# Optimization experiments

Hardware: AMD Instinct MI355X
Metric: run time of the kernel (lower is better)

## Reference

```python
import jax, jax.numpy as jnp
import numpy as np

NUM_HEADS = 12
SIZE_PER_HEAD = 64
NEG_INF = -10000.0


def setup_inputs() -> dict:
    key = jax.random.key(0)
    k1, k2, k3, k4 = jax.random.split(key, 4)
    B, S, D = 2, 2048, 768
    x = jax.random.normal(k1, (B, S, D), dtype=jnp.float32)
    mask = jax.random.randint(k2, (B, S, S), 0, 2, dtype=jnp.int32)
    std = 0.02
    Wq = jax.random.normal(k3, (D, NUM_HEADS * SIZE_PER_HEAD), dtype=jnp.float32) * std
    Wk = jax.random.normal(k4, (D, NUM_HEADS * SIZE_PER_HEAD), dtype=jnp.float32) * std
    bq = jnp.zeros((NUM_HEADS * SIZE_PER_HEAD,), dtype=jnp.float32)
    bk = jnp.zeros((NUM_HEADS * SIZE_PER_HEAD,), dtype=jnp.float32)
    return {"x": x, "mask": mask, "Wq": Wq, "bq": bq, "Wk": Wk, "bk": bk}


def reference(x, mask, Wq, bq, Wk, bk):
    B, S, D = x.shape
    H, dh = NUM_HEADS, SIZE_PER_HEAD
    # Dense query/key projections (no activation), then split heads: [B,H,S,dh]
    q = (x @ Wq + bq).reshape(B, S, H, dh).transpose(0, 2, 1, 3)
    k = (x @ Wk + bk).reshape(B, S, H, dh).transpose(0, 2, 1, 3)
    # Scaled dot-product scores: [B,H,S,S]
    scores = jnp.einsum("bhqd,bhkd->bhqk", q, k) / jnp.sqrt(jnp.float32(dh))
    # Mask: [B,S,S] -> [B,1,S,S]; zeros get large negative additive bias
    adder = (1.0 - mask.astype(jnp.float32))[:, None, :, :] * NEG_INF
    probs = jax.nn.softmax(scores + adder, axis=-1)
    # dropout is identity at inference (training=None)
    return probs
```

## Files before the change

### kernel.cpp

```cpp
#include <hip/hip_runtime.h>
#include <stdint.h>

#define NUM_HEADS 12
#define DH 64
#define SEQ 2048
#define BATCH 2
#define DM 768
#define NQK 1536
#define LOG2E 1.44269504088896340736f

typedef short short8 __attribute__((ext_vector_type(8)));
typedef short short4_t __attribute__((ext_vector_type(4)));
typedef float f32x4 __attribute__((ext_vector_type(4)));

__device__ __forceinline__ short bf16_rne(float f) {
    union { float f; uint32_t u; } v; v.f = f;
    return (short)((v.u + 0x7FFFu + ((v.u >> 16) & 1u)) >> 16);
}

__global__ __launch_bounds__(256) void wt_kernel(const float* __restrict__ Wq,
                                                 const float* __restrict__ Wk,
                                                 short* __restrict__ Wt) {
    __shared__ float tile[32][33];
    int n0 = blockIdx.x * 32;
    int k0 = blockIdx.y * 32;
    int tx = threadIdx.x & 31;
    int ty = threadIdx.x >> 5;
    const float* src = (n0 < DM) ? Wq : Wk;
    int nn0 = (n0 < DM) ? n0 : n0 - DM;
#pragma unroll
    for (int j = 0; j < 4; ++j) {
        int k = ty + 8 * j;
        tile[k][tx] = src[(size_t)(k0 + k) * DM + nn0 + tx];
    }
    __syncthreads();
#pragma unroll
    for (int j = 0; j < 4; ++j) {
        int n = ty + 8 * j;
        Wt[(size_t)(n0 + n) * DM + k0 + tx] = bf16_rne(tile[tx][n]);
    }
}

__global__ __launch_bounds__(256) void xb_kernel(const float* __restrict__ x,
                                                 short* __restrict__ Xb) {
    int i = (blockIdx.x * 256 + threadIdx.x) * 4;
    f32x4 v = *(const f32x4*)(x + i);
    short4_t s;
#pragma unroll
    for (int j = 0; j < 4; ++j) s[j] = bf16_rne(v[j]);
    *(short4_t*)(Xb + i) = s;
}

__global__ __launch_bounds__(256) void mpack_kernel(const int* __restrict__ mask,
                                                    unsigned long long* __restrict__ Mb) {
    int wid = (blockIdx.x * 256 + threadIdx.x) >> 6;
    int lane = threadIdx.x & 63;
    size_t base = (size_t)wid * 8;
#pragma unroll
    for (int i = 0; i < 8; ++i) {
        size_t w = base + i;
        int v = mask[w * 64 + lane];
        unsigned long long bal = __ballot(v != 0);
        if (lane == 0) Mb[w] = bal;
    }
}

__global__ __launch_bounds__(256) void proj_kernel(const short* __restrict__ Xb,
                                                   const short* __restrict__ Wt,
                                                   const float* __restrict__ bq,
                                                   const float* __restrict__ bk,
                                                   short* __restrict__ QK) {
    __shared__ short As[128 * 40];
    __shared__ short Bs[128 * 40];
    const int m0 = blockIdx.x * 128;
    const int n0 = blockIdx.y * 128;
    const int t = threadIdx.x;
    const int lane = t & 63;
    const int w = t >> 6;
    const int wr = w >> 1, wc = w & 1;
    const int lr = lane & 15;
    const int lk = lane >> 4;

    f32x4 acc[4][4] = {};

    for (int k0 = 0; k0 < DM; k0 += 32) {
#pragma unroll
        for (int j = 0; j < 2; ++j) {
            int idx = t + 256 * j;
            int row = idx >> 2;
            int ch = idx & 3;
            *(short8*)&As[row * 40 + ch * 8] =
                *(const short8*)&Xb[(size_t)(m0 + row) * DM + k0 + ch * 8];
            *(short8*)&Bs[row * 40 + ch * 8] =
                *(const short8*)&Wt[(size_t)(n0 + row) * DM + k0 + ch * 8];
        }
        __syncthreads();
        short8 a[4], bfr[4];
#pragma unroll
        for (int m = 0; m < 4; ++m)
            a[m] = *(short8*)&As[(wr * 64 + m * 16 + lr) * 40 + lk * 8];
#pragma unroll
        for (int n = 0; n < 4; ++n)
            bfr[n] = *(short8*)&Bs[(wc * 64 + n * 16 + lr) * 40 + lk * 8];
#pragma unroll
        for (int m = 0; m < 4; ++m)
#pragma unroll
            for (int n = 0; n < 4; ++n)
                acc[m][n] = __builtin_amdgcn_mfma_f32_16x16x32_bf16(a[m], bfr[n], acc[m][n], 0, 0, 0);
        __syncthreads();
    }

    const int orow = m0 + wr * 64;
    const int ocol = n0 + wc * 64;
#pragma unroll
    for (int m = 0; m < 4; ++m) {
#pragma unroll
        for (int n = 0; n < 4; ++n) {
            int col = ocol + n * 16 + lr;
            float bias = (col < DM) ? bq[col] : bk[col - DM];
            float scale = (col < DM) ? 0.125f * LOG2E : 1.0f;
#pragma unroll
            for (int r = 0; r < 4; ++r) {
                int row = orow + m * 16 + lk * 4 + r;
                QK[(size_t)row * NQK + col] = bf16_rne((acc[m][n][r] + bias) * scale);
            }
        }
    }
}

__global__ __launch_bounds__(256) void attn_kernel(const short* __restrict__ QK,
                                                   const unsigned long long* __restrict__ Mb,
                                                   float* __restrict__ out) {
    __shared__ short Ks[64 * 72];
    const int qblk = blockIdx.x;
    const int h = blockIdx.y;
    const int b = blockIdx.z;
    const int t = threadIdx.x;
    const int lane = t & 63;
    const int w = t >> 6;
    const int lr = lane & 15;
    const int lk = lane >> 4;
    const int wq = qblk * 64 + w * 16;

    short8 aq[2];
#pragma unroll
    for (int ks = 0; ks < 2; ++ks)
        aq[ks] = *(const short8*)&QK[(size_t)(b * SEQ + wq + lr) * NQK + h * DH + ks * 32 + lk * 8];

    float lrow[4] = {0.f, 0.f, 0.f, 0.f};
    const size_t mrow0 = (size_t)b * SEQ * (SEQ / 64);

    for (int kt = 0; kt < SEQ; kt += 64) {
#pragma unroll
        for (int j = 0; j < 2; ++j) {
            int idx = t + 256 * j;
            int row = idx >> 3;
            int ch = idx & 7;
            *(short8*)&Ks[row * 72 + ch * 8] =
                *(const short8*)&QK[(size_t)(b * SEQ + kt + row) * NQK + DM + h * DH + ch * 8];
        }
        __syncthreads();
        f32x4 sc[4];
#pragma unroll
        for (int nf = 0; nf < 4; ++nf) {
            short8 k0 = *(short8*)&Ks[(nf * 16 + lr) * 72 + lk * 8];
            short8 k1 = *(short8*)&Ks[(nf * 16 + lr) * 72 + 32 + lk * 8];
            f32x4 a = {0.f, 0.f, 0.f, 0.f};
            a = __builtin_amdgcn_mfma_f32_16x16x32_bf16(aq[0], k0, a, 0, 0, 0);
            a = __builtin_amdgcn_mfma_f32_16x16x32_bf16(aq[1], k1, a, 0, 0, 0);
            sc[nf] = a;
        }
#pragma unroll
        for (int r = 0; r < 4; ++r) {
            int q = wq + lk * 4 + r;
            unsigned long long mbs = Mb[mrow0 + (size_t)q * 32 + (kt >> 6)] >> lr;
            float s = 0.f;
#pragma unroll
            for (int nf = 0; nf < 4; ++nf) {
                float e = __builtin_amdgcn_exp2f(sc[nf][r]);
                s += ((mbs >> (nf * 16)) & 1ull) ? e : 0.f;
            }
            lrow[r] += s;
        }
        __syncthreads();
    }

    float inv[4];
#pragma unroll
    for (int r = 0; r < 4; ++r) {
        float l = lrow[r];
        l += __shfl_xor(l, 1, 64);
        l += __shfl_xor(l, 2, 64);
        l += __shfl_xor(l, 4, 64);
        l += __shfl_xor(l, 8, 64);
        inv[r] = 1.0f / l;
    }

    for (int kt = 0; kt < SEQ; kt += 64) {
#pragma unroll
        for (int j = 0; j < 2; ++j) {
            int idx = t + 256 * j;
            int row = idx >> 3;
            int ch = idx & 7;
            *(short8*)&Ks[row * 72 + ch * 8] =
                *(const short8*)&QK[(size_t)(b * SEQ + kt + row) * NQK + DM + h * DH + ch * 8];
        }
        __syncthreads();
        f32x4 sc[4];
#pragma unroll
        for (int nf = 0; nf < 4; ++nf) {
            short8 k0 = *(short8*)&Ks[(nf * 16 + lr) * 72 + lk * 8];
            short8 k1 = *(short8*)&Ks[(nf * 16 + lr) * 72 + 32 + lk * 8];
            f32x4 a = {0.f, 0.f, 0.f, 0.f};
            a = __builtin_amdgcn_mfma_f32_16x16x32_bf16(aq[0], k0, a, 0, 0, 0);
            a = __builtin_amdgcn_mfma_f32_16x16x32_bf16(aq[1], k1, a, 0, 0, 0);
            sc[nf] = a;
        }
#pragma unroll
        for (int r = 0; r < 4; ++r) {
            int q = wq + lk * 4 + r;
            unsigned long long mbs = Mb[mrow0 + (size_t)q * 32 + (kt >> 6)] >> lr;
            float* op = &out[((size_t)((b * NUM_HEADS + h) * SEQ + q)) * SEQ + kt + lr];
#pragma unroll
            for (int nf = 0; nf < 4; ++nf) {
                float p = __builtin_amdgcn_exp2f(sc[nf][r]) * inv[r];
                op[nf * 16] = ((mbs >> (nf * 16)) & 1ull) ? p : 0.f;
            }
        }
        __syncthreads();
    }
}

extern "C" void kernel_launch(void* const* d_in, const int* in_sizes, int n_in,
                              void* d_out, int out_size, void* d_ws, size_t ws_size,
                              hipStream_t stream) {
    (void)in_sizes; (void)n_in; (void)out_size; (void)ws_size;
    const float* x = (const float*)d_in[0];
    const int* mask = (const int*)d_in[1];
    const float* Wq = (const float*)d_in[2];
    const float* bq = (const float*)d_in[3];
    const float* Wk = (const float*)d_in[4];
    const float* bk = (const float*)d_in[5];
    float* out = (float*)d_out;

    short* Wt = (short*)d_ws;
    short* Xb = Wt + (size_t)NQK * DM;
    short* QK = Xb + (size_t)BATCH * SEQ * DM;
    unsigned long long* Mb =
        (unsigned long long*)(QK + (size_t)BATCH * SEQ * NQK);

    wt_kernel<<<dim3(NQK / 32, DM / 32), 256, 0, stream>>>(Wq, Wk, Wt);
    xb_kernel<<<dim3((BATCH * SEQ * DM) / (256 * 4)), 256, 0, stream>>>(x, Xb);
    mpack_kernel<<<dim3((BATCH * SEQ * SEQ / 64) / 32), 256, 0, stream>>>(mask, Mb);
    proj_kernel<<<dim3(BATCH * SEQ / 128, NQK / 128), 256, 0, stream>>>(Xb, Wt, bq, bk, QK);
    attn_kernel<<<dim3(SEQ / 64, NUM_HEADS, BATCH), 256, 0, stream>>>(QK, Mb, out);
}
```

Baseline: 173.0 us.

## Double-buffer projection and attention tiles, transpose score MFMA for vector stores

The projection GEMM tile shrinks to 128x64 and both kernels get register-staged double-buffered shared memory, so the next K tile is fetched while MFMAs run on the current one. The attention kernel swaps the MFMA operands so each lane holds four consecutive key columns of one query row. That allows 16-byte vectorized output stores and a single mask word per lane. The 1/rowsum normalization is folded into the exponent by seeding the accumulator with -log2(sum), which removes a multiply but adds more shared memory per block.

Result: slower. 186.7 us (+7.9%).

```diff
diff --git a/kernel.cpp b/kernel.cpp
--- a/kernel.cpp
+++ b/kernel.cpp
@@ -70,10 +70,10 @@
                                                    const float* __restrict__ bq,
                                                    const float* __restrict__ bk,
                                                    short* __restrict__ QK) {
-    __shared__ short As[128 * 40];
-    __shared__ short Bs[128 * 40];
+    __shared__ short As[2][128 * 40];
+    __shared__ short Bs[2][64 * 40];
     const int m0 = blockIdx.x * 128;
-    const int n0 = blockIdx.y * 128;
+    const int n0 = blockIdx.y * 64;
     const int t = threadIdx.x;
     const int lane = t & 63;
     const int w = t >> 6;
@@ -81,41 +81,52 @@
     const int lr = lane & 15;
     const int lk = lane >> 4;
 
-    f32x4 acc[4][4] = {};
-
-    for (int k0 = 0; k0 < DM; k0 += 32) {
-#pragma unroll
-        for (int j = 0; j < 2; ++j) {
-            int idx = t + 256 * j;
-            int row = idx >> 2;
-            int ch = idx & 3;
-            *(short8*)&As[row * 40 + ch * 8] =
-                *(const short8*)&Xb[(size_t)(m0 + row) * DM + k0 + ch * 8];
-            *(short8*)&Bs[row * 40 + ch * 8] =
-                *(const short8*)&Wt[(size_t)(n0 + row) * DM + k0 + ch * 8];
-        }
+    const int ar0 = t >> 2, ach = t & 3;
+    const int br0 = t >> 2, bch = t & 3;
+
+    f32x4 acc[4][2] = {};
+    short8 ra0, ra1, rb;
+
+#define PROJ_LOAD(K0)                                                              \
+    ra0 = *(const short8*)&Xb[(size_t)(m0 + ar0) * DM + (K0) + ach * 8];           \
+    ra1 = *(const short8*)&Xb[(size_t)(m0 + ar0 + 64) * DM + (K0) + ach * 8];      \
+    rb  = *(const short8*)&Wt[(size_t)(n0 + br0) * DM + (K0) + bch * 8];
+
+#define PROJ_WRITE(BUF)                                                            \
+    *(short8*)&As[BUF][ar0 * 40 + ach * 8] = ra0;                                  \
+    *(short8*)&As[BUF][(ar0 + 64) * 40 + ach * 8] = ra1;                           \
+    *(short8*)&Bs[BUF][br0 * 40 + bch * 8] = rb;
+
+    PROJ_LOAD(0)
+    PROJ_WRITE(0)
+    __syncthreads();
+
+    int cur = 0;
+    for (int s = 0; s < DM / 32; ++s) {
+        if (s < DM / 32 - 1) { PROJ_LOAD((s + 1) * 32) }
+        short8 a[4], bb[2];
+#pragma unroll
+        for (int m = 0; m < 4; ++m)
+            a[m] = *(short8*)&As[cur][(wr * 64 + m * 16 + lr) * 40 + lk * 8];
+#pragma unroll
+        for (int n = 0; n < 2; ++n)
+            bb[n] = *(short8*)&Bs[cur][(wc * 32 + n * 16 + lr) * 40 + lk * 8];
+#pragma unroll
+        for (int m = 0; m < 4; ++m)
+#pragma unroll
+            for (int n = 0; n < 2; ++n)
+                acc[m][n] = __builtin_amdgcn_mfma_f32_16x16x32_bf16(a[m], bb[n], acc[m][n], 0, 0, 0);
+        if (s < DM / 32 - 1) { PROJ_WRITE(cur ^ 1) }
         __syncthreads();
-        short8 a[4], bfr[4];
-#pragma unroll
-        for (int m = 0; m < 4; ++m)
-            a[m] = *(short8*)&As[(wr * 64 + m * 16 + lr) * 40 + lk * 8];
-#pragma unroll
-        for (int n = 0; n < 4; ++n)
-            bfr[n] = *(short8*)&Bs[(wc * 64 + n * 16 + lr) * 40 + lk * 8];
-#pragma unroll
-        for (int m = 0; m < 4; ++m)
-#pragma unroll
-            for (int n = 0; n < 4; ++n)
-                acc[m][n] = __builtin_amdgcn_mfma_f32_16x16x32_bf16(a[m], bfr[n], acc[m][n], 0, 0, 0);
-        __syncthreads();
+        cur ^= 1;
     }
 
     const int orow = m0 + wr * 64;
-    const int ocol = n0 + wc * 64;
+    const int ocol = n0 + wc * 32;
 #pragma unroll
     for (int m = 0; m < 4; ++m) {
 #pragma unroll
-        for (int n = 0; n < 4; ++n) {
+        for (int n = 0; n < 2; ++n) {
             int col = ocol + n * 16 + lr;
             float bias = (col < DM) ? bq[col] : bk[col - DM];
             float scale = (col < DM) ? 0.125f * LOG2E : 1.0f;
@@ -126,12 +137,14 @@
             }
         }
     }
+#undef PROJ_LOAD
+#undef PROJ_WRITE
 }
 
 __global__ __launch_bounds__(256) void attn_kernel(const short* __restrict__ QK,
                                                    const unsigned long long* __restrict__ Mb,
                                                    float* __restrict__ out) {
-    __shared__ short Ks[64 * 72];
+    __shared__ short Ks[2][64 * 72];
     const int qblk = blockIdx.x;
     const int h = blockIdx.y;
     const int b = blockIdx.z;
@@ -141,94 +154,82 @@
     const int lr = lane & 15;
     const int lk = lane >> 4;
     const int wq = qblk * 64 + w * 16;
-
-    short8 aq[2];
-#pragma unroll
-    for (int ks = 0; ks < 2; ++ks)
-        aq[ks] = *(const short8*)&QK[(size_t)(b * SEQ + wq + lr) * NQK + h * DH + ks * 32 + lk * 8];
-
-    float lrow[4] = {0.f, 0.f, 0.f, 0.f};
-    const size_t mrow0 = (size_t)b * SEQ * (SEQ / 64);
-
+    const int q = wq + lr;
+
+    short8 aq0 = *(const short8*)&QK[(size_t)(b * SEQ + q) * NQK + h * DH + lk * 8];
+    short8 aq1 = *(const short8*)&QK[(size_t)(b * SEQ + q) * NQK + h * DH + 32 + lk * 8];
+
+    const size_t mrow = (size_t)b * SEQ * (SEQ / 64) + (size_t)q * 32;
+    const int srow = t >> 3, sch = t & 7;
+    short8 rs0, rs1;
+
+#define ATT_LOAD(KT)                                                                          \
+    rs0 = *(const short8*)&QK[(size_t)(b * SEQ + (KT) + srow) * NQK + DM + h * DH + sch * 8]; \
+    rs1 = *(const short8*)&QK[(size_t)(b * SEQ + (KT) + srow + 32) * NQK + DM + h * DH + sch * 8];
+
+#define ATT_WRITE(BUF)                                                                        \
+    *(short8*)&Ks[BUF][srow * 72 + sch * 8] = rs0;                                            \
+    *(short8*)&Ks[BUF][(srow + 32) * 72 + sch * 8] = rs1;
+
+    float lsum = 0.0f;
+    ATT_LOAD(0)
+    ATT_WRITE(0)
+    __syncthreads();
+    int cur = 0;
     for (int kt = 0; kt < SEQ; kt += 64) {
-#pragma unroll
-        for (int j = 0; j < 2; ++j) {
-            int idx = t + 256 * j;
-            int row = idx >> 3;
-            int ch = idx & 7;
-            *(short8*)&Ks[row * 72 + ch * 8] =
-                *(const short8*)&QK[(size_t)(b * SEQ + kt + row) * NQK + DM + h * DH + ch * 8];
-        }
-        __syncthreads();
-        f32x4 sc[4];
+        if (kt + 64 < SEQ) { ATT_LOAD(kt + 64) }
+        unsigned long long mbs = Mb[mrow + (kt >> 6)] >> (lk * 4);
 #pragma unroll
         for (int nf = 0; nf < 4; ++nf) {
-            short8 k0 = *(short8*)&Ks[(nf * 16 + lr) * 72 + lk * 8];
-            short8 k1 = *(short8*)&Ks[(nf * 16 + lr) * 72 + 32 + lk * 8];
+            short8 k0 = *(short8*)&Ks[cur][(nf * 16 + lr) * 72 + lk * 8];
+            short8 k1 = *(short8*)&Ks[cur][(nf * 16 + lr) * 72 + 32 + lk * 8];
             f32x4 a = {0.f, 0.f, 0.f, 0.f};
-            a = __builtin_amdgcn_mfma_f32_16x16x32_bf16(aq[0], k0, a, 0, 0, 0);
-            a = __builtin_amdgcn_mfma_f32_16x16x32_bf16(aq[1], k1, a, 0, 0, 0);
-            sc[nf] = a;
-        }
-#pragma unroll
-        for (int r = 0; r < 4; ++r) {
-            int q = wq + lk * 4 + r;
-            unsigned long long mbs = Mb[mrow0 + (size_t)q * 32 + (kt >> 6)] >> lr;
-            float s = 0.f;
-#pragma unroll
-            for (int nf = 0; nf < 4; ++nf) {
-                float e = __builtin_amdgcn_exp2f(sc[nf][r]);
-                s += ((mbs >> (nf * 16)) & 1ull) ? e : 0.f;
-            }
-            lrow[r] += s;
-        }
-        __syncthreads();
-    }
-
-    float inv[4];
-#pragma unroll
-    for (int r = 0; r < 4; ++r) {
-        float l = lrow[r];
-        l += __shfl_xor(l, 1, 64);
-        l += __shfl_xor(l, 2, 64);
-        l += __shfl_xor(l, 4, 64);
-        l += __shfl_xor(l, 8, 64);
-        inv[r] = 1.0f / l;
-    }
-
-    for (int kt = 0; kt < SEQ; kt += 64) {
-#pragma unroll
-        for (int j = 0; j < 2; ++j) {
-            int idx = t + 256 * j;
-            int row = idx >> 3;
-            int ch = idx & 7;
-            *(short8*)&Ks[row * 72 + ch * 8] =
-                *(const short8*)&QK[(size_t)(b * SEQ + kt + row) * NQK + DM + h * DH + ch * 8];
-        }
-        __syncthreads();
-        f32x4 sc[4];
-#pragma unroll
-        for (int nf = 0; nf < 4; ++nf) {
-            short8 k0 = *(short8*)&Ks[(nf * 16 + lr) * 72 + lk * 8];
-            short8 k1 = *(short8*)&Ks[(nf * 16 + lr) * 72 + 32 + lk * 8];
-            f32x4 a = {0.f, 0.f, 0.f, 0.f};
-            a = __builtin_amdgcn_mfma_f32_16x16x32_bf16(aq[0], k0, a, 0, 0, 0);
-            a = __builtin_amdgcn_mfma_f32_16x16x32_bf16(aq[1], k1, a, 0, 0, 0);
-            sc[nf] = a;
-        }
-#pragma unroll
-        for (int r = 0; r < 4; ++r) {
-            int q = wq + lk * 4 + r;
-            unsigned long long mbs = Mb[mrow0 + (size_t)q * 32 + (kt >> 6)] >> lr;
-            float* op = &out[((size_t)((b * NUM_HEADS + h) * SEQ + q)) * SEQ + kt + lr];
-#pragma unroll
-            for (int nf = 0; nf < 4; ++nf) {
-                float p = __builtin_amdgcn_exp2f(sc[nf][r]) * inv[r];
-                op[nf * 16] = ((mbs >> (nf * 16)) & 1ull) ? p : 0.f;
+            a = __builtin_amdgcn_mfma_f32_16x16x32_bf16(k0, aq0, a, 0, 0, 0);
+            a = __builtin_amdgcn_mfma_f32_16x16x32_bf16(k1, aq1, a, 0, 0, 0);
+#pragma unroll
+            for (int r = 0; r < 4; ++r) {
+                float e = __builtin_amdgcn_exp2f(a[r]);
+                lsum += ((mbs >> (nf * 16 + r)) & 1ull) ? e : 0.f;
             }
         }
+        if (kt + 64 < SEQ) { ATT_WRITE(cur ^ 1) }
         __syncthreads();
-    }
+        cur ^= 1;
+    }
+
+    lsum += __shfl_xor(lsum, 16, 64);
+    lsum += __shfl_xor(lsum, 32, 64);
+    float li = -__log2f(lsum);
+    f32x4 li4 = {li, li, li, li};
+
+    const size_t orow = ((size_t)((b * NUM_HEADS + h) * SEQ) + q) * SEQ;
+    ATT_LOAD(0)
+    ATT_WRITE(0)
+    __syncthreads();
+    cur = 0;
+    for (int kt = 0; kt < SEQ; kt += 64) {
+        if (kt + 64 < SEQ) { ATT_LOAD(kt + 64) }
+        unsigned long long mbs = Mb[mrow + (kt >> 6)] >> (lk * 4);
+#pragma unroll
+        for (int nf = 0; nf < 4; ++nf) {
+            short8 k0 = *(short8*)&Ks[cur][(nf * 16 + lr) * 72 + lk * 8];
+            short8 k1 = *(short8*)&Ks[cur][(nf * 16 + lr) * 72 + 32 + lk * 8];
+            f32x4 a = __builtin_amdgcn_mfma_f32_16x16x32_bf16(k0, aq0, li4, 0, 0, 0);
+            a = __builtin_amdgcn_mfma_f32_16x16x32_bf16(k1, aq1, a, 0, 0, 0);
+            f32x4 p;
+#pragma unroll
+            for (int r = 0; r < 4; ++r) {
+                float e = __builtin_amdgcn_exp2f(a[r]);
+                p[r] = ((mbs >> (nf * 16 + r)) & 1ull) ? e : 0.f;
+            }
+            *(f32x4*)&out[orow + kt + nf * 16 + lk * 4] = p;
+        }
+        if (kt + 64 < SEQ) { ATT_WRITE(cur ^ 1) }
+        __syncthreads();
+        cur ^= 1;
+    }
+#undef ATT_LOAD
+#undef ATT_WRITE
 }
 
 extern "C" void kernel_launch(void* const* d_in, const int* in_sizes, int n_in,
@@ -252,6 +253,6 @@
     wt_kernel<<<dim3(NQK / 32, DM / 32), 256, 0, stream>>>(Wq, Wk, Wt);
     xb_kernel<<<dim3((BATCH * SEQ * DM) / (256 * 4)), 256, 0, stream>>>(x, Xb);
     mpack_kernel<<<dim3((BATCH * SEQ * SEQ / 64) / 32), 256, 0, stream>>>(mask, Mb);
-    proj_kernel<<<dim3(BATCH * SEQ / 128, NQK / 128), 256, 0, stream>>>(Xb, Wt, bq, bk, QK);
+    proj_kernel<<<dim3(BATCH * SEQ / 128, NQK / 64), 256, 0, stream>>>(Xb, Wt, bq, bk, QK);
     attn_kernel<<<dim3(SEQ / 64, NUM_HEADS, BATCH), 256, 0, stream>>>(QK, Mb, out);
 }
```
